# Kernel tuning notes

Hardware: AMD Instinct MI355X
Metric: run time of the kernel (lower is better)

The kernel has to match this reference:

```python
import jax, jax.numpy as jnp
import numpy as np

N_NODES = 100000
N_EDGES = 3200000
IN_F, HID, OUT_F = 128, 3, 4


def setup_inputs() -> dict:
    key = jax.random.key(0)
    k1, k2, k3, k4, k5, k6 = jax.random.split(key, 6)
    x = jax.random.normal(k1, (N_NODES, IN_F), dtype=jnp.float32)
    edge_index = jax.random.randint(k2, (2, N_EDGES), 0, N_NODES, dtype=jnp.int64)
    # GCNConv weight (glorot) + bias, Linear(3,4) weight + bias
    W = jax.random.normal(k3, (IN_F, HID), dtype=jnp.float32) * (1.0 / np.sqrt(IN_F))
    b = jnp.zeros((HID,), dtype=jnp.float32)
    Wout = jax.random.normal(k4, (HID, OUT_F), dtype=jnp.float32) * (1.0 / np.sqrt(HID))
    bout = jax.random.normal(k5, (OUT_F,), dtype=jnp.float32) * 0.01
    return {"x": x, "edge_index": edge_index, "W": W, "b": b, "Wout": Wout, "bout": bout}


def reference(x, edge_index, W, b, Wout, bout):
    N = x.shape[0]
    # add self loops (PyG GCNConv default: add_self_loops=True)
    loop = jnp.arange(N, dtype=edge_index.dtype)
    row = jnp.concatenate([edge_index[0], loop])  # source nodes
    col = jnp.concatenate([edge_index[1], loop])  # destination nodes
    # linear transform first (cheaper: 128 -> 3)
    xw = x @ W  # [N, 3]
    # symmetric degree normalization: deg computed on destination index
    deg = jax.ops.segment_sum(jnp.ones_like(col, dtype=x.dtype), col, num_segments=N)
    dinv = jnp.where(deg > 0, jax.lax.rsqrt(deg), 0.0)
    norm = dinv[row] * dinv[col]  # [E+N]
    # gather source features, scale, scatter-add to destinations
    msg = xw[row] * norm[:, None]  # [E+N, 3]
    agg = jax.ops.segment_sum(msg, col, num_segments=N)  # [N, 3]
    h = jax.nn.relu(agg + b)
    z = h @ Wout + bout
    return (h, z)
```

## Files before the change

### kernel.cpp

```cpp
#include <hip/hip_runtime.h>

#define N_NODES 100000
#define N_EDGES 3200000
#define IN_F    128
#define HID     3
#define OUT_F   4

#define BSHIFT  7
#define BSIZE   128
#define NBUCK   ((N_NODES + BSIZE - 1) / BSIZE)
#define NBLKA   512
#define EPB     ((N_EDGES + NBLKA - 1) / NBLKA)
#define NH      (NBUCK * NBLKA)

#define SCAN_ITEMS 16
#define SCAN_BLOCK 256
#define SCAN_PER_BLOCK (SCAN_ITEMS * SCAN_BLOCK)
#define NS1 ((NH + SCAN_PER_BLOCK - 1) / SCAN_PER_BLOCK)


__device__ inline float wave_reduce_sum(float v) {
    #pragma unroll
    for (int off = 32; off > 0; off >>= 1)
        v += __shfl_down(v, off, 64);
    return v;
}

__global__ void xw_kernel(const float* __restrict__ x,
                          const float* __restrict__ W,
                          float* __restrict__ xw) {
    int wave = threadIdx.x >> 6;
    int lane = threadIdx.x & 63;
    int node = blockIdx.x * 4 + wave;
    if (node >= N_NODES) return;

    float2 xv = *reinterpret_cast<const float2*>(x + (size_t)node * IN_F + lane * 2);
    const float* w = W + (lane * 2) * HID;
    float s0 = xv.x * w[0] + xv.y * w[3];
    float s1 = xv.x * w[1] + xv.y * w[4];
    float s2 = xv.x * w[2] + xv.y * w[5];
    s0 = wave_reduce_sum(s0);
    s1 = wave_reduce_sum(s1);
    s2 = wave_reduce_sum(s2);
    if (lane == 0) {
        xw[node * 3 + 0] = s0;
        xw[node * 3 + 1] = s1;
        xw[node * 3 + 2] = s2;
    }
}

__global__ void histA_kernel(const int* __restrict__ col, int* __restrict__ histG) {
    __shared__ int hist[NBUCK];
    int tid = threadIdx.x, blk = blockIdx.x;
    for (int i = tid; i < NBUCK; i += 256) hist[i] = 0;
    __syncthreads();
    int start = blk * EPB, end = min(start + EPB, N_EDGES);
    for (int e = start + tid; e < end; e += 256)
        atomicAdd(&hist[col[e] >> BSHIFT], 1);
    __syncthreads();
    for (int i = tid; i < NBUCK; i += 256)
        histG[i * NBLKA + blk] = hist[i];
}

__global__ void scan1_kernel(int* __restrict__ data, int* __restrict__ bsum) {
    __shared__ int s[SCAN_BLOCK];
    int tid = threadIdx.x;
    int base = blockIdx.x * SCAN_PER_BLOCK + tid * SCAN_ITEMS;
    int v[SCAN_ITEMS];
    int tsum = 0;
    #pragma unroll
    for (int j = 0; j < SCAN_ITEMS; ++j) {
        v[j] = (base + j < NH) ? data[base + j] : 0;
        tsum += v[j];
    }
    s[tid] = tsum;
    __syncthreads();
    for (int off = 1; off < SCAN_BLOCK; off <<= 1) {
        int t = (tid >= off) ? s[tid - off] : 0;
        __syncthreads();
        s[tid] += t;
        __syncthreads();
    }
    int run = s[tid] - tsum;
    #pragma unroll
    for (int j = 0; j < SCAN_ITEMS; ++j) {
        int t = v[j];
        if (base + j < NH) data[base + j] = run;
        run += t;
    }
    if (tid == SCAN_BLOCK - 1) bsum[blockIdx.x] = s[SCAN_BLOCK - 1];
}

__global__ void scan2_kernel(int* __restrict__ bsum) {
    __shared__ int s[SCAN_BLOCK];
    int tid = threadIdx.x;
    int v = (tid < NS1) ? bsum[tid] : 0;
    s[tid] = v;
    __syncthreads();
    for (int off = 1; off < SCAN_BLOCK; off <<= 1) {
        int t = (tid >= off) ? s[tid - off] : 0;
        __syncthreads();
        s[tid] += t;
        __syncthreads();
    }
    if (tid < NS1) bsum[tid] = s[tid] - v;
}

__global__ void scan3_kernel(int* __restrict__ data, const int* __restrict__ bsum) {
    int i = blockIdx.x * blockDim.x + threadIdx.x;
    if (i < NH) data[i] += bsum[i / SCAN_PER_BLOCK];
}

__global__ void fillB_kernel(const int* __restrict__ row,
                             const int* __restrict__ col,
                             const int* __restrict__ histG,
                             int* __restrict__ packed) {
    __shared__ int offs[NBUCK];
    int tid = threadIdx.x, blk = blockIdx.x;
    for (int i = tid; i < NBUCK; i += 256) offs[i] = histG[i * NBLKA + blk];
    __syncthreads();
    int start = blk * EPB, end = min(start + EPB, N_EDGES);
    for (int e = start + tid; e < end; e += 256) {
        int c = col[e], r = row[e];
        int b = c >> BSHIFT;
        int pos = atomicAdd(&offs[b], 1);
        packed[pos] = (r << BSHIFT) | (c & (BSIZE - 1));
    }
}

__global__ void degC_kernel(const int* __restrict__ histG,
                            const int* __restrict__ packed,
                            float* __restrict__ dinv) {
    __shared__ int cnt[BSIZE];
    int tid = threadIdx.x, b = blockIdx.x;
    if (tid < BSIZE) cnt[tid] = 0;
    __syncthreads();
    int start = histG[b * NBLKA];
    int end   = (b + 1 < NBUCK) ? histG[(b + 1) * NBLKA] : N_EDGES;
    for (int i = start + tid; i < end; i += 256)
        atomicAdd(&cnt[packed[i] & (BSIZE - 1)], 1);
    __syncthreads();
    if (tid < BSIZE) {
        int node = b * BSIZE + tid;
        if (node < N_NODES) dinv[node] = rsqrtf((float)(cnt[tid] + 1));
    }
}

__global__ void xwn_kernel(const float* __restrict__ xw,
                           const float* __restrict__ dinv,
                           float4* __restrict__ xwn4) {
    int i = blockIdx.x * blockDim.x + threadIdx.x;
    if (i < N_NODES) {
        float d = dinv[i];
        xwn4[i] = make_float4(xw[i * 3 + 0] * d, xw[i * 3 + 1] * d,
                              xw[i * 3 + 2] * d, 0.f);
    }
}

__global__ void aggC_kernel(const int* __restrict__ histG,
                            const int* __restrict__ packed,
                            const float4* __restrict__ xwn4,
                            const float* __restrict__ dinv,
                            const float* __restrict__ bb,
                            const float* __restrict__ Wout,
                            const float* __restrict__ bout,
                            float* __restrict__ out) {
    __shared__ float acc[BSIZE * 3];
    int tid = threadIdx.x, b = blockIdx.x;
    for (int i = tid; i < BSIZE * 3; i += 256) acc[i] = 0.f;
    __syncthreads();
    int start = histG[b * NBLKA];
    int end   = (b + 1 < NBUCK) ? histG[(b + 1) * NBLKA] : N_EDGES;
    for (int i = start + tid; i < end; i += 256) {
        int p  = packed[i];
        int r  = p >> BSHIFT;
        int cl = p & (BSIZE - 1);
        float4 v = xwn4[r];
        atomicAdd(&acc[cl * 3 + 0], v.x);
        atomicAdd(&acc[cl * 3 + 1], v.y);
        atomicAdd(&acc[cl * 3 + 2], v.z);
    }
    __syncthreads();
    if (tid < BSIZE) {
        int node = b * BSIZE + tid;
        if (node < N_NODES) {
            float di = dinv[node];
            float4 s = xwn4[node];
            float h0 = fmaxf((acc[tid * 3 + 0] + s.x) * di + bb[0], 0.f);
            float h1 = fmaxf((acc[tid * 3 + 1] + s.y) * di + bb[1], 0.f);
            float h2 = fmaxf((acc[tid * 3 + 2] + s.z) * di + bb[2], 0.f);
            out[node * 3 + 0] = h0;
            out[node * 3 + 1] = h1;
            out[node * 3 + 2] = h2;
            float* z = out + (size_t)N_NODES * 3;
            #pragma unroll
            for (int k = 0; k < 4; ++k) {
                z[node * 4 + k] = bout[k] + h0 * Wout[0 * 4 + k]
                                          + h1 * Wout[1 * 4 + k]
                                          + h2 * Wout[2 * 4 + k];
            }
        }
    }
}

extern "C" void kernel_launch(void* const* d_in, const int* in_sizes, int n_in,
                              void* d_out, int out_size, void* d_ws, size_t ws_size,
                              hipStream_t stream) {
    const float* x    = (const float*)d_in[0];
    const int*   ei   = (const int*)d_in[1];
    const float* W    = (const float*)d_in[2];
    const float* b    = (const float*)d_in[3];
    const float* Wout = (const float*)d_in[4];
    const float* bout = (const float*)d_in[5];
    float* out = (float*)d_out;

    char* wsb = (char*)d_ws;
    int*    histG  = (int*)(wsb);
    int*    packed = (int*)(wsb + (size_t)NH * 4);
    float*  xw     = (float*)(wsb + (size_t)NH * 4 + (size_t)N_EDGES * 4);
    float4* xwn4   = (float4*)((char*)xw + (size_t)N_NODES * 3 * 4);
    float*  dinv   = (float*)((char*)xwn4 + (size_t)N_NODES * 16);
    int*    bsum   = (int*)((char*)dinv + (size_t)N_NODES * 4);

    const int* row = ei;
    const int* col = ei + N_EDGES;

    const int B = 256;
    int gridN  = (N_NODES + B - 1) / B;
    int gridX  = (N_NODES + 3) / 4;
    int gridS3 = (NH + B - 1) / B;

    xw_kernel<<<gridX, B, 0, stream>>>(x, W, xw);
    histA_kernel<<<NBLKA, B, 0, stream>>>(col, histG);
    scan1_kernel<<<NS1, SCAN_BLOCK, 0, stream>>>(histG, bsum);
    scan2_kernel<<<1, SCAN_BLOCK, 0, stream>>>(bsum);
    scan3_kernel<<<gridS3, B, 0, stream>>>(histG, bsum);
    fillB_kernel<<<NBLKA, B, 0, stream>>>(row, col, histG, packed);
    degC_kernel<<<NBUCK, B, 0, stream>>>(histG, packed, dinv);
    xwn_kernel<<<gridN, B, 0, stream>>>(xw, dinv, xwn4);
    aggC_kernel<<<NBUCK, B, 0, stream>>>(histG, packed, xwn4, dinv, b, Wout, bout, out);
}
```

Baseline: 260.5 us.

## Fuse degree normalization into degree kernel, widen blocks and unroll edge loops

The separate xwn kernel is folded into the degree kernel, which now writes the normalized features with dinv stored in the fourth float4 lane, so the aggregation kernel no longer reads a dinv array. The degree and aggregation kernels move to 512-thread blocks and unroll their edge loops four-wide to keep more gathers in flight. The xw kernel now uses float4 loads with half-wave reductions, handling two nodes per wave. This removes one launch and some global traffic, at the cost of more register pressure and a more complex tail loop.

After: 233.1 us. 10.5% less time.

```diff
diff --git a/kernel.cpp b/kernel.cpp
--- a/kernel.cpp
+++ b/kernel.cpp
@@ -19,30 +19,28 @@
 #define NS1 ((NH + SCAN_PER_BLOCK - 1) / SCAN_PER_BLOCK)
 
 
-__device__ inline float wave_reduce_sum(float v) {
-    #pragma unroll
-    for (int off = 32; off > 0; off >>= 1)
-        v += __shfl_down(v, off, 64);
-    return v;
-}
-
 __global__ void xw_kernel(const float* __restrict__ x,
                           const float* __restrict__ W,
                           float* __restrict__ xw) {
     int wave = threadIdx.x >> 6;
     int lane = threadIdx.x & 63;
-    int node = blockIdx.x * 4 + wave;
+    int half = lane >> 5;
+    int l    = lane & 31;
+    int node = blockIdx.x * 8 + wave * 2 + half;
     if (node >= N_NODES) return;
 
-    float2 xv = *reinterpret_cast<const float2*>(x + (size_t)node * IN_F + lane * 2);
-    const float* w = W + (lane * 2) * HID;
-    float s0 = xv.x * w[0] + xv.y * w[3];
-    float s1 = xv.x * w[1] + xv.y * w[4];
-    float s2 = xv.x * w[2] + xv.y * w[5];
-    s0 = wave_reduce_sum(s0);
-    s1 = wave_reduce_sum(s1);
-    s2 = wave_reduce_sum(s2);
-    if (lane == 0) {
+    float4 xv = *reinterpret_cast<const float4*>(x + (size_t)node * IN_F + l * 4);
+    const float* w = W + l * 4 * HID;
+    float s0 = xv.x * w[0] + xv.y * w[3] + xv.z * w[6] + xv.w * w[9];
+    float s1 = xv.x * w[1] + xv.y * w[4] + xv.z * w[7] + xv.w * w[10];
+    float s2 = xv.x * w[2] + xv.y * w[5] + xv.z * w[8] + xv.w * w[11];
+    #pragma unroll
+    for (int off = 16; off > 0; off >>= 1) {
+        s0 += __shfl_down(s0, off, 32);
+        s1 += __shfl_down(s1, off, 32);
+        s2 += __shfl_down(s2, off, 32);
+    }
+    if (l == 0) {
         xw[node * 3 + 0] = s0;
         xw[node * 3 + 1] = s1;
         xw[node * 3 + 2] = s2;
@@ -128,64 +126,87 @@
     }
 }
 
-__global__ void degC_kernel(const int* __restrict__ histG,
-                            const int* __restrict__ packed,
-                            float* __restrict__ dinv) {
+__global__ __launch_bounds__(512) void degC_kernel(const int* __restrict__ histG,
+                                                   const int* __restrict__ packed,
+                                                   const float* __restrict__ xw,
+                                                   float4* __restrict__ xwn4) {
     __shared__ int cnt[BSIZE];
     int tid = threadIdx.x, b = blockIdx.x;
     if (tid < BSIZE) cnt[tid] = 0;
     __syncthreads();
     int start = histG[b * NBLKA];
     int end   = (b + 1 < NBUCK) ? histG[(b + 1) * NBLKA] : N_EDGES;
-    for (int i = start + tid; i < end; i += 256)
-        atomicAdd(&cnt[packed[i] & (BSIZE - 1)], 1);
-    __syncthreads();
-    if (tid < BSIZE) {
-        int node = b * BSIZE + tid;
-        if (node < N_NODES) dinv[node] = rsqrtf((float)(cnt[tid] + 1));
-    }
-}
-
-__global__ void xwn_kernel(const float* __restrict__ xw,
-                           const float* __restrict__ dinv,
-                           float4* __restrict__ xwn4) {
-    int i = blockIdx.x * blockDim.x + threadIdx.x;
-    if (i < N_NODES) {
-        float d = dinv[i];
-        xwn4[i] = make_float4(xw[i * 3 + 0] * d, xw[i * 3 + 1] * d,
-                              xw[i * 3 + 2] * d, 0.f);
-    }
-}
-
-__global__ void aggC_kernel(const int* __restrict__ histG,
-                            const int* __restrict__ packed,
-                            const float4* __restrict__ xwn4,
-                            const float* __restrict__ dinv,
-                            const float* __restrict__ bb,
-                            const float* __restrict__ Wout,
-                            const float* __restrict__ bout,
-                            float* __restrict__ out) {
-    __shared__ float acc[BSIZE * 3];
-    int tid = threadIdx.x, b = blockIdx.x;
-    for (int i = tid; i < BSIZE * 3; i += 256) acc[i] = 0.f;
-    __syncthreads();
-    int start = histG[b * NBLKA];
-    int end   = (b + 1 < NBUCK) ? histG[(b + 1) * NBLKA] : N_EDGES;
-    for (int i = start + tid; i < end; i += 256) {
-        int p  = packed[i];
-        int r  = p >> BSHIFT;
-        int cl = p & (BSIZE - 1);
-        float4 v = xwn4[r];
-        atomicAdd(&acc[cl * 3 + 0], v.x);
-        atomicAdd(&acc[cl * 3 + 1], v.y);
-        atomicAdd(&acc[cl * 3 + 2], v.z);
-    }
+    int len   = end - start;
+    int nfull = len & ~(4 * 512 - 1);
+    for (int off = tid; off < nfull; off += 2048) {
+        int p0 = packed[start + off];
+        int p1 = packed[start + off + 512];
+        int p2 = packed[start + off + 1024];
+        int p3 = packed[start + off + 1536];
+        atomicAdd(&cnt[p0 & (BSIZE - 1)], 1);
+        atomicAdd(&cnt[p1 & (BSIZE - 1)], 1);
+        atomicAdd(&cnt[p2 & (BSIZE - 1)], 1);
+        atomicAdd(&cnt[p3 & (BSIZE - 1)], 1);
+    }
+    for (int off = nfull + tid; off < len; off += 512)
+        atomicAdd(&cnt[packed[start + off] & (BSIZE - 1)], 1);
     __syncthreads();
     if (tid < BSIZE) {
         int node = b * BSIZE + tid;
         if (node < N_NODES) {
-            float di = dinv[node];
+            float d = rsqrtf((float)(cnt[tid] + 1));
+            xwn4[node] = make_float4(xw[node * 3 + 0] * d,
+                                     xw[node * 3 + 1] * d,
+                                     xw[node * 3 + 2] * d, d);
+        }
+    }
+}
+
+__global__ __launch_bounds__(512) void aggC_kernel(const int* __restrict__ histG,
+                                                   const int* __restrict__ packed,
+                                                   const float4* __restrict__ xwn4,
+                                                   const float* __restrict__ bb,
+                                                   const float* __restrict__ Wout,
+                                                   const float* __restrict__ bout,
+                                                   float* __restrict__ out) {
+    __shared__ float acc[BSIZE * 3];
+    int tid = threadIdx.x, b = blockIdx.x;
+    for (int i = tid; i < BSIZE * 3; i += 512) acc[i] = 0.f;
+    __syncthreads();
+    int start = histG[b * NBLKA];
+    int end   = (b + 1 < NBUCK) ? histG[(b + 1) * NBLKA] : N_EDGES;
+    int len   = end - start;
+    int nfull = len & ~(4 * 512 - 1);
+    for (int off = tid; off < nfull; off += 2048) {
+        int p0 = packed[start + off];
+        int p1 = packed[start + off + 512];
+        int p2 = packed[start + off + 1024];
+        int p3 = packed[start + off + 1536];
+        float4 v0 = xwn4[p0 >> BSHIFT];
+        float4 v1 = xwn4[p1 >> BSHIFT];
+        float4 v2 = xwn4[p2 >> BSHIFT];
+        float4 v3 = xwn4[p3 >> BSHIFT];
+        int c0 = (p0 & (BSIZE - 1)) * 3, c1 = (p1 & (BSIZE - 1)) * 3;
+        int c2 = (p2 & (BSIZE - 1)) * 3, c3 = (p3 & (BSIZE - 1)) * 3;
+        atomicAdd(&acc[c0 + 0], v0.x); atomicAdd(&acc[c0 + 1], v0.y); atomicAdd(&acc[c0 + 2], v0.z);
+        atomicAdd(&acc[c1 + 0], v1.x); atomicAdd(&acc[c1 + 1], v1.y); atomicAdd(&acc[c1 + 2], v1.z);
+        atomicAdd(&acc[c2 + 0], v2.x); atomicAdd(&acc[c2 + 1], v2.y); atomicAdd(&acc[c2 + 2], v2.z);
+        atomicAdd(&acc[c3 + 0], v3.x); atomicAdd(&acc[c3 + 1], v3.y); atomicAdd(&acc[c3 + 2], v3.z);
+    }
+    for (int off = nfull + tid; off < len; off += 512) {
+        int p = packed[start + off];
+        float4 v = xwn4[p >> BSHIFT];
+        int c = (p & (BSIZE - 1)) * 3;
+        atomicAdd(&acc[c + 0], v.x);
+        atomicAdd(&acc[c + 1], v.y);
+        atomicAdd(&acc[c + 2], v.z);
+    }
+    __syncthreads();
+    if (tid < BSIZE) {
+        int node = b * BSIZE + tid;
+        if (node < N_NODES) {
             float4 s = xwn4[node];
+            float di = s.w;
             float h0 = fmaxf((acc[tid * 3 + 0] + s.x) * di + bb[0], 0.f);
             float h1 = fmaxf((acc[tid * 3 + 1] + s.y) * di + bb[1], 0.f);
             float h2 = fmaxf((acc[tid * 3 + 2] + s.z) * di + bb[2], 0.f);
@@ -219,15 +240,13 @@
     int*    packed = (int*)(wsb + (size_t)NH * 4);
     float*  xw     = (float*)(wsb + (size_t)NH * 4 + (size_t)N_EDGES * 4);
     float4* xwn4   = (float4*)((char*)xw + (size_t)N_NODES * 3 * 4);
-    float*  dinv   = (float*)((char*)xwn4 + (size_t)N_NODES * 16);
-    int*    bsum   = (int*)((char*)dinv + (size_t)N_NODES * 4);
+    int*    bsum   = (int*)((char*)xwn4 + (size_t)N_NODES * 16);
 
     const int* row = ei;
     const int* col = ei + N_EDGES;
 
     const int B = 256;
-    int gridN  = (N_NODES + B - 1) / B;
-    int gridX  = (N_NODES + 3) / 4;
+    int gridX  = (N_NODES + 7) / 8;
     int gridS3 = (NH + B - 1) / B;
 
     xw_kernel<<<gridX, B, 0, stream>>>(x, W, xw);
@@ -236,7 +255,6 @@
     scan2_kernel<<<1, SCAN_BLOCK, 0, stream>>>(bsum);
     scan3_kernel<<<gridS3, B, 0, stream>>>(histG, bsum);
     fillB_kernel<<<NBLKA, B, 0, stream>>>(row, col, histG, packed);
-    degC_kernel<<<NBUCK, B, 0, stream>>>(histG, packed, dinv);
-    xwn_kernel<<<gridN, B, 0, stream>>>(xw, dinv, xwn4);
-    aggC_kernel<<<NBUCK, B, 0, stream>>>(histG, packed, xwn4, dinv, b, Wout, bout, out);
-}
+    degC_kernel<<<NBUCK, 512, 0, stream>>>(histG, packed, xw, xwn4);
+    aggC_kernel<<<NBUCK, 512, 0, stream>>>(histG, packed, xwn4, b, Wout, bout, out);
+}
```
